# Kernel optimization log

Measured on AMD Instinct MI355X. Metric: run time of the kernel, lower is better.

The kernel has to match this reference:

```python
import jax, jax.numpy as jnp
import numpy as np
import math

DN = ('NCHW', 'OIHW', 'NCHW')

def conv2d(x, w, b=None, pad=0):
    y = jax.lax.conv_general_dilated(x, w, (1, 1), [(pad, pad), (pad, pad)], dimension_numbers=DN)
    if b is not None:
        y = y + b[None, :, None, None]
    return y

def group_norm(x, weight, bias, groups=32, eps=1e-5):
    B, C, H, W = x.shape
    xg = x.reshape(B, groups, C // groups, H, W)
    mean = xg.mean(axis=(2, 3, 4), keepdims=True)
    var = xg.var(axis=(2, 3, 4), keepdims=True)
    xg = (xg - mean) * jax.lax.rsqrt(var + eps)
    return xg.reshape(B, C, H, W) * weight[None, :, None, None] + bias[None, :, None, None]

def swish(x):
    return x * jax.nn.sigmoid(x)

def setup_inputs() -> dict:
    key = jax.random.key(0)
    ks = jax.random.split(key, 20)
    B, C, H, W = 8, 192, 48, 48
    emb = 192
    n_div = 12
    Cq = C // n_div  # 16
    s = 0.02
    return {
        'x': jax.random.normal(ks[0], (B, C, H, W), jnp.float32),
        'xe': jax.random.normal(ks[1], (B, C, H, W), jnp.float32),
        'time_emb': jax.random.normal(ks[2], (B, emb), jnp.float32),
        'gn1_w': jnp.ones((C,), jnp.float32),
        'gn1_b': jnp.zeros((C,), jnp.float32),
        'conv1_w': jax.random.normal(ks[3], (C, C, 3, 3), jnp.float32) * s,
        'conv1_b': jnp.zeros((C,), jnp.float32),
        'aff_w': jax.random.normal(ks[4], (2 * C, emb), jnp.float32) * s,
        'aff_b': jnp.zeros((2 * C,), jnp.float32),
        'gn2_w': jnp.ones((C,), jnp.float32),
        'gn2_b': jnp.zeros((C,), jnp.float32),
        'conv2_w': jax.random.normal(ks[5], (C, C, 3, 3), jnp.float32) * s,
        'conv2_b': jnp.zeros((C,), jnp.float32),
        'q_w': jax.random.normal(ks[6], (Cq, C, 1, 1), jnp.float32) * s,
        'kv_w': jax.random.normal(ks[7], (2 * Cq, C, 1, 1), jnp.float32) * s,
        'out_w': jax.random.normal(ks[8], (C, Cq, 3, 3), jnp.float32) * s,
        'out_b': jnp.zeros((C,), jnp.float32),
    }

def reference(x, xe, time_emb, gn1_w, gn1_b, conv1_w, conv1_b, aff_w, aff_b,
              gn2_w, gn2_b, conv2_w, conv2_b, q_w, kv_w, out_w, out_b):
    B, C, H, W = x.shape
    n_head, n_div = 1, 12
    head_dim = C // (n_head * n_div)

    # ----- ResnetBlock -----
    h = conv2d(swish(group_norm(x, gn1_w, gn1_b)), conv1_w, conv1_b, pad=1)
    # FeatureWiseAffine (use_affine_level=True)
    gb = time_emb @ aff_w.T + aff_b          # [B, 2C]
    gamma, beta = jnp.split(gb, 2, axis=1)   # each [B, C]
    gb_sum = 0.5 * (gamma + beta)[:, :, None, None]
    h = h + gb_sum * h + gb_sum
    h = conv2d(swish(group_norm(h, gn2_w, gn2_b)), conv2_w, conv2_b, pad=1)
    xres = h + x  # res_conv is Identity (dim == dim_out)

    # ----- CrossAttention -----
    Ye, Xe = xe.shape[-2], xe.shape[-1]
    query = conv2d(xres, q_w).reshape(B, n_head, head_dim, H, W)
    kv = conv2d(xe, kv_w).reshape(B, n_head, head_dim * 2, Ye, Xe)
    key_, value = jnp.split(kv, 2, axis=2)
    scale = 1.0 / math.sqrt(C // n_div)
    attn = jnp.einsum('bnchw,bncyx->bnhwyx', query, key_) * scale
    attn = jax.nn.softmax(attn.reshape(B, n_head, H, W, -1), axis=-1)
    attn = attn.reshape(B, n_head, H, W, Ye, Xe)
    out = jnp.einsum('bnhwyx,bncyx->bnchw', attn, value)
    out = conv2d(out.reshape(B, C // n_div, H, W), out_w, out_b, pad=1)
    return out + xres
```

## Files before the change

kernel.cpp:

```cpp
#include <hip/hip_runtime.h>
#include <hip/hip_bf16.h>

#define NB 8
#define NC 192
#define NH 48
#define NW 48
#define NP 2304
#define NGROUPS 32
#define CPG 6
#define NEMB 192
#define NCQ 16

#define PH 50
#define PWS 52
#define ACT_T_ELEMS ((size_t)NB * PH * PWS * NC)
#define AOT_ELEMS   ((size_t)NB * PH * PWS * 16)

typedef __attribute__((ext_vector_type(4))) short s16x4;
typedef __attribute__((ext_vector_type(8))) short s16x8;
typedef __attribute__((ext_vector_type(4))) float f32x4;

static __device__ inline short f2bf(float v) {
  __hip_bfloat16 h = __float2bfloat16(v);
  return *(short*)&h;
}

__global__ __launch_bounds__(256) void wprep_kernel(const float* __restrict__ w,
                                                    short* __restrict__ wbuf) {
  int i = blockIdx.x * 256 + threadIdx.x;
  if (i >= 6 * 9 * 12 * 64 * 8) return;
  int j  = i & 7;
  int l  = (i >> 3) & 63;
  int cf = (i >> 9) % 12;
  int tk = (i >> 9) / 12;
  int t  = tk % 9;
  int kc = tk / 9;
  int co = cf * 16 + (l & 15);
  int ci = kc * 32 + (l >> 4) * 8 + j;
  wbuf[i] = f2bf(w[((size_t)co * NC + ci) * 9 + t]);
}

__global__ __launch_bounds__(256) void wprep_o_kernel(const float* __restrict__ w,
                                                      short* __restrict__ wbuf) {
  int i = blockIdx.x * 256 + threadIdx.x;
  if (i >= 9 * 12 * 64 * 8) return;
  int j  = i & 7;
  int l  = (i >> 3) & 63;
  int cf = (i >> 9) % 12;
  int t  = (i >> 9) / 12;
  int co = cf * 16 + (l & 15);
  int ci = (l >> 4) * 8 + j;
  wbuf[i] = (ci < 16) ? f2bf(w[((size_t)co * 16 + ci) * 9 + t]) : (short)0;
}

__global__ __launch_bounds__(256) void affine_kernel(const float* __restrict__ emb,
                                                     const float* __restrict__ aw,
                                                     const float* __restrict__ ab,
                                                     float* __restrict__ gbsum) {
  int i = blockIdx.x * 256 + threadIdx.x;
  if (i >= NB * NC) return;
  int b = i / NC;
  int c = i - b * NC;
  const float* e  = emb + b * NEMB;
  const float* w0 = aw + c * NEMB;
  const float* w1 = aw + (c + NC) * NEMB;
  float s = 0.f;
  for (int j = 0; j < NEMB; ++j) s += e[j] * (w0[j] + w1[j]);
  gbsum[i] = 0.5f * (s + ab[c] + ab[c + NC]);
}

__global__ __launch_bounds__(256) void halo_zero_kernel(short* __restrict__ actt) {
  int b = blockIdx.y;
  int i = blockIdx.x * 256 + threadIdx.x;
  if (i >= 9600) return;
  int c4 = i % 48;
  int r  = i / 48;
  size_t off;
  if (r < 52)       off = ((size_t)0 * PWS + r) * NC;
  else if (r < 104) off = ((size_t)49 * PWS + (r - 52)) * NC;
  else if (r < 152) off = ((size_t)(r - 104 + 1) * PWS + 0) * NC;
  else              off = ((size_t)(r - 152 + 1) * PWS + 49) * NC;
  *(s16x4*)(&actt[(size_t)b * PH * PWS * NC + off + c4 * 4]) = (s16x4){0, 0, 0, 0};
}

__global__ __launch_bounds__(256) void halo_zero16_kernel(short* __restrict__ aot) {
  int b = blockIdx.x;
  for (int i = threadIdx.x; i < 784; i += 256) {
    int c4  = i & 3;
    int pos = i >> 2;
    int r, col;
    if (pos < 50)       { r = 0;  col = pos; }
    else if (pos < 100) { r = 49; col = pos - 50; }
    else if (pos < 148) { r = pos - 100 + 1; col = 0; }
    else                { r = pos - 148 + 1; col = 49; }
    *(s16x4*)(&aot[(((size_t)b * PH + r) * PWS + col) * 16 + c4 * 4]) = (s16x4){0, 0, 0, 0};
  }
}

__global__ __launch_bounds__(256) void gn_stats_kernel(const float* __restrict__ in,
                                                       float* __restrict__ stats) {
  int bg = blockIdx.x;
  const float4* p = (const float4*)(in + (size_t)bg * (CPG * NP));
  float s = 0.f, s2 = 0.f;
  for (int i = threadIdx.x; i < CPG * NP / 4; i += 256) {
    float4 v = p[i];
    s  += v.x + v.y + v.z + v.w;
    s2 += v.x * v.x + v.y * v.y + v.z * v.z + v.w * v.w;
  }
#pragma unroll
  for (int off = 32; off > 0; off >>= 1) {
    s  += __shfl_down(s, off);
    s2 += __shfl_down(s2, off);
  }
  __shared__ float red[8];
  int wave = threadIdx.x >> 6;
  if ((threadIdx.x & 63) == 0) { red[wave * 2] = s; red[wave * 2 + 1] = s2; }
  __syncthreads();
  if (threadIdx.x == 0) {
    float S  = red[0] + red[2] + red[4] + red[6];
    float S2 = red[1] + red[3] + red[5] + red[7];
    const float invN = 1.f / (float)(CPG * NP);
    float mean = S * invN;
    float var  = S2 * invN - mean * mean;
    stats[bg * 2]     = mean;
    stats[bg * 2 + 1] = rsqrtf(var + 1e-5f);
  }
}

__global__ __launch_bounds__(256) void gn_apply_t_kernel(const float* __restrict__ in,
                                                         const float* __restrict__ stats,
                                                         const float* __restrict__ gw,
                                                         const float* __restrict__ gb,
                                                         short* __restrict__ actt) {
  __shared__ float tile[48 * 193];
  int bh = blockIdx.x;
  int b = bh / NH;
  int h = bh - b * NH;
  int tid = threadIdx.x;
  for (int i = tid; i < 2304; i += 256) {
    int c = i / 12;
    int w = (i % 12) * 4;
    float4 v = *(const float4*)(in + (((size_t)b * NC + c) * NH + h) * NW + w);
    float mean = stats[(b * NGROUPS + c / CPG) * 2];
    float rstd = stats[(b * NGROUPS + c / CPG) * 2 + 1];
    float sc = rstd * gw[c];
    float sh = gb[c] - mean * sc;
    float y;
    y = v.x * sc + sh; tile[(w + 0) * 193 + c] = y / (1.f + __expf(-y));
    y = v.y * sc + sh; tile[(w + 1) * 193 + c] = y / (1.f + __expf(-y));
    y = v.z * sc + sh; tile[(w + 2) * 193 + c] = y / (1.f + __expf(-y));
    y = v.w * sc + sh; tile[(w + 3) * 193 + c] = y / (1.f + __expf(-y));
  }
  __syncthreads();
  short* dst = actt + (((size_t)b * PH + h + 1) * PWS + 1) * NC;
  for (int i = tid; i < 2304; i += 256) {
    int w  = i / 48;
    int c4 = (i - w * 48) * 4;
    s16x4 o;
    o.x = f2bf(tile[w * 193 + c4 + 0]);
    o.y = f2bf(tile[w * 193 + c4 + 1]);
    o.z = f2bf(tile[w * 193 + c4 + 2]);
    o.w = f2bf(tile[w * 193 + c4 + 3]);
    *(s16x4*)(dst + (size_t)w * NC + c4) = o;
  }
}

template <bool AFFINE, bool RESID>
__global__ __launch_bounds__(256) void conv_mfma_kernel(const short* __restrict__ actt,
                                                        const short* __restrict__ wbuf,
                                                        const float* __restrict__ bias,
                                                        const float* __restrict__ gbsum,
                                                        const float* __restrict__ resid,
                                                        float* __restrict__ out) {
  __shared__ short S[4][50][40];
  int bs = blockIdx.x;
  int b = bs / 24;
  int strip = bs - b * 24;
  int coB = blockIdx.y;
  int h0 = strip * 2;
  int tid = threadIdx.x;
  int lane = tid & 63, wave = tid >> 6;
  int wy = wave >> 1, wx = wave & 1;
  int g8 = (lane >> 4) * 8;

  f32x4 acc[2][3];
#pragma unroll
  for (int m = 0; m < 2; ++m)
#pragma unroll
    for (int f = 0; f < 3; ++f) acc[m][f] = (f32x4){0.f, 0.f, 0.f, 0.f};

  const size_t actbase = ((size_t)b * PH + h0) * PWS * NC;

  for (int kc = 0; kc < 6; ++kc) {
    __syncthreads();
    for (int i = tid; i < 800; i += 256) {
      int ci8 = i & 3;
      int rc  = i >> 2;
      int col = rc % 50, r = rc / 50;
      const s16x8* src = (const s16x8*)(actt + actbase + ((size_t)r * PWS + col) * NC +
                                        kc * 32 + ci8 * 8);
      *(s16x8*)(&S[r][col][ci8 * 8]) = *src;
    }
    __syncthreads();
#pragma unroll
    for (int t = 0; t < 9; ++t) {
      int ky = t / 3, kx = t - ky * 3;
      const short* wp = wbuf + ((((size_t)kc * 9 + t) * 12 + (coB * 4 + wy * 2)) * 64 + lane) * 8;
      s16x8 a0 = *(const s16x8*)wp;
      s16x8 a1 = *(const s16x8*)(wp + 64 * 8);
      int row = wx + ky;
#pragma unroll
      for (int f = 0; f < 3; ++f) {
        int col = f * 16 + (lane & 15) + kx;
        s16x8 bf = *(const s16x8*)(&S[row][col][g8]);
        acc[0][f] = __builtin_amdgcn_mfma_f32_16x16x32_bf16(a0, bf, acc[0][f], 0, 0, 0);
        acc[1][f] = __builtin_amdgcn_mfma_f32_16x16x32_bf16(a1, bf, acc[1][f], 0, 0, 0);
      }
    }
  }
  int hout = h0 + wx;
#pragma unroll
  for (int m = 0; m < 2; ++m) {
    int co0 = coB * 64 + wy * 32 + m * 16;
#pragma unroll
    for (int r = 0; r < 4; ++r) {
      int co = co0 + (lane >> 4) * 4 + r;
      float bv = bias[co];
      float s = AFFINE ? gbsum[b * NC + co] : 0.f;
#pragma unroll
      for (int f = 0; f < 3; ++f) {
        int w = f * 16 + (lane & 15);
        size_t o = (((size_t)b * NC + co) * NH + hout) * NW + w;
        float v = acc[m][f][r] + bv;
        if (AFFINE) v = v * (1.f + s) + s;
        if (RESID) v += resid[o];
        out[o] = v;
      }
    }
  }
}

__global__ __launch_bounds__(256) void out_conv_mfma_kernel(const short* __restrict__ aot,
                                                            const short* __restrict__ wbuf,
                                                            const float* __restrict__ bias,
                                                            float* __restrict__ out) {
  __shared__ short S[4][50][40];
  int bs = blockIdx.x;
  int b = bs / 24;
  int strip = bs - b * 24;
  int coB = blockIdx.y;
  int h0 = strip * 2;
  int tid = threadIdx.x;
  int lane = tid & 63, wave = tid >> 6;
  int wy = wave >> 1, wx = wave & 1;
  int g8 = (lane >> 4) * 8;

  f32x4 acc[2][3];
#pragma unroll
  for (int m = 0; m < 2; ++m)
#pragma unroll
    for (int f = 0; f < 3; ++f) acc[m][f] = (f32x4){0.f, 0.f, 0.f, 0.f};

  const size_t base = ((size_t)b * PH + h0) * PWS * 16;
  for (int i = tid; i < 800; i += 256) {
    int ci8 = i & 3;
    int rc  = i >> 2;
    int col = rc % 50, r = rc / 50;
    s16x8 v = (s16x8){0, 0, 0, 0, 0, 0, 0, 0};
    if (ci8 < 2)
      v = *(const s16x8*)(aot + base + ((size_t)r * PWS + col) * 16 + ci8 * 8);
    *(s16x8*)(&S[r][col][ci8 * 8]) = v;
  }
  __syncthreads();
#pragma unroll
  for (int t = 0; t < 9; ++t) {
    int ky = t / 3, kx = t - ky * 3;
    const short* wp = wbuf + (((size_t)t * 12 + (coB * 4 + wy * 2)) * 64 + lane) * 8;
    s16x8 a0 = *(const s16x8*)wp;
    s16x8 a1 = *(const s16x8*)(wp + 64 * 8);
    int row = wx + ky;
#pragma unroll
    for (int f = 0; f < 3; ++f) {
      int col = f * 16 + (lane & 15) + kx;
      s16x8 bf = *(const s16x8*)(&S[row][col][g8]);
      acc[0][f] = __builtin_amdgcn_mfma_f32_16x16x32_bf16(a0, bf, acc[0][f], 0, 0, 0);
      acc[1][f] = __builtin_amdgcn_mfma_f32_16x16x32_bf16(a1, bf, acc[1][f], 0, 0, 0);
    }
  }
  int hout = h0 + wx;
#pragma unroll
  for (int m = 0; m < 2; ++m) {
    int co0 = coB * 64 + wy * 32 + m * 16;
#pragma unroll
    for (int r = 0; r < 4; ++r) {
      int co = co0 + (lane >> 4) * 4 + r;
      float bv = bias[co];
#pragma unroll
      for (int f = 0; f < 3; ++f) {
        int w = f * 16 + (lane & 15);
        size_t o = (((size_t)b * NC + co) * NH + hout) * NW + w;
        out[o] = acc[m][f][r] + bv + out[o];
      }
    }
  }
}

template <int NOUT>
__global__ __launch_bounds__(256) void prep_partial_kernel(const float* __restrict__ X,
                                                           const float* __restrict__ W,
                                                           float* __restrict__ part) {
  __shared__ float wl[NOUT][64];
  int pt = blockIdx.x, ch = blockIdx.y, b = blockIdx.z;
  for (int i = threadIdx.x; i < NOUT * 64; i += 256) {
    int o = i >> 6, c = i & 63;
    wl[o][c] = W[o * NC + ch * 64 + c];
  }
  __syncthreads();
  int p = pt * 256 + threadIdx.x;
  const float* ip = X + ((size_t)b * NC + ch * 64) * NP + p;
  float acc[NOUT];
#pragma unroll
  for (int o = 0; o < NOUT; ++o) acc[o] = 0.f;
#pragma unroll 8
  for (int ci = 0; ci < 64; ++ci) {
    float xv = ip[(size_t)ci * NP];
#pragma unroll
    for (int o = 0; o < NOUT; ++o) acc[o] += xv * wl[o][ci];
  }
  float* op = part + ((size_t)(ch * NB + b) * NOUT) * NP + p;
#pragma unroll
  for (int o = 0; o < NOUT; ++o) op[(size_t)o * NP] = acc[o];
}

__global__ __launch_bounds__(256) void prep_pack_kernel(const float* __restrict__ pq,
                                                        const float* __restrict__ pkv,
                                                        short* __restrict__ Qb,
                                                        short* __restrict__ Kb,
                                                        short* __restrict__ VTb) {
  __shared__ short QL[16][264], KL[16][264];
  int pt = blockIdx.x, b = blockIdx.y;
  int tp = threadIdx.x;
  int p  = pt * 256 + tp;
  const float SC = 0.36067376022224085f;
#pragma unroll
  for (int o = 0; o < 16; ++o) {
    float s = pq[((size_t)(0 * NB + b) * 16 + o) * NP + p] +
              pq[((size_t)(1 * NB + b) * 16 + o) * NP + p] +
              pq[((size_t)(2 * NB + b) * 16 + o) * NP + p];
    QL[o][tp] = f2bf(s * SC);
  }
#pragma unroll
  for (int o = 0; o < 32; ++o) {
    float s = pkv[((size_t)(0 * NB + b) * 32 + o) * NP + p] +
              pkv[((size_t)(1 * NB + b) * 32 + o) * NP + p] +
              pkv[((size_t)(2 * NB + b) * 32 + o) * NP + p];
    if (o < 16) KL[o][tp] = f2bf(s);
    else VTb[((size_t)b * 16 + (o - 16)) * NP + p] = f2bf(s);
  }
  __syncthreads();
  short* qp = Qb + ((size_t)b * NP + p) * 32;
  short* kp = Kb + ((size_t)b * NP + p) * 32;
#pragma unroll
  for (int o4 = 0; o4 < 4; ++o4) {
    s16x4 vq = {QL[o4 * 4 + 0][tp], QL[o4 * 4 + 1][tp], QL[o4 * 4 + 2][tp], QL[o4 * 4 + 3][tp]};
    s16x4 vk = {KL[o4 * 4 + 0][tp], KL[o4 * 4 + 1][tp], KL[o4 * 4 + 2][tp], KL[o4 * 4 + 3][tp]};
    *(s16x4*)(qp + o4 * 4) = vq;
    *(s16x4*)(kp + o4 * 4) = vk;
    *(s16x4*)(qp + 16 + o4 * 4) = (s16x4){0, 0, 0, 0};
    *(s16x4*)(kp + 16 + o4 * 4) = (s16x4){0, 0, 0, 0};
  }
}

__global__ __launch_bounds__(1024) void attn_mfma_kernel(const short* __restrict__ Qb,
                                                         const short* __restrict__ Kb,
                                                         const short* __restrict__ VTb,
                                                         short* __restrict__ aot) {
  __shared__ float PM[4][4][64], PL[4][4][64];
  __shared__ f32x4 PA[4][4][64];
  int b    = blockIdx.y;
  int tid  = threadIdx.x;
  int lane = tid & 63;
  int w    = tid >> 6;
  int qg   = w & 3, ks = w >> 2;
  int q0   = blockIdx.x * 64 + qg * 16;
  int g    = lane >> 4;
  int ql   = lane & 15;

  s16x8 qfrag = *(const s16x8*)(Qb + ((size_t)b * NP + q0 + ql) * 32 + g * 8);

  int r0 = 8 * (ql >> 2) + (ql & 3);
  const short* Kbase = Kb + (size_t)b * NP * 32 + g * 8;
  const short* Vbase = VTb + ((size_t)b * 16 + ql) * NP;

  f32x4 acc = {0.f, 0.f, 0.f, 0.f};
  float m = -1e30f, l = 0.f;

  int kk = ks * 576;
  s16x8 kf0 = *(const s16x8*)(Kbase + (size_t)(kk + r0) * 32);
  s16x8 kf1 = *(const s16x8*)(Kbase + (size_t)(kk + r0 + 4) * 32);
  s16x8 vf  = *(const s16x8*)(Vbase + kk + g * 8);

  for (int step = 0; step < 18; ++step) {
    int kn = (step < 17) ? kk + 32 : ks * 576;
    s16x8 nk0 = *(const s16x8*)(Kbase + (size_t)(kn + r0) * 32);
    s16x8 nk1 = *(const s16x8*)(Kbase + (size_t)(kn + r0 + 4) * 32);
    s16x8 nv  = *(const s16x8*)(Vbase + kn + g * 8);

    f32x4 z = {0.f, 0.f, 0.f, 0.f};
    f32x4 s0 = __builtin_amdgcn_mfma_f32_16x16x32_bf16(kf0, qfrag, z, 0, 0, 0);
    f32x4 s1 = __builtin_amdgcn_mfma_f32_16x16x32_bf16(kf1, qfrag, z, 0, 0, 0);

    float tm = fmaxf(fmaxf(fmaxf(s0[0], s0[1]), fmaxf(s0[2], s0[3])),
                     fmaxf(fmaxf(s1[0], s1[1]), fmaxf(s1[2], s1[3])));
    if (!__all(tm <= m + 8.0f)) {
      tm = fmaxf(tm, __shfl_xor(tm, 16, 64));
      tm = fmaxf(tm, __shfl_xor(tm, 32, 64));
      float mn = fmaxf(m, tm);
      float corr = exp2f(m - mn);
      m = mn;
      l *= corr;
      acc[0] *= corr; acc[1] *= corr; acc[2] *= corr; acc[3] *= corr;
    }
    float p0 = exp2f(s0[0] - m), p1 = exp2f(s0[1] - m);
    float p2 = exp2f(s0[2] - m), p3 = exp2f(s0[3] - m);
    float p4 = exp2f(s1[0] - m), p5 = exp2f(s1[1] - m);
    float p6 = exp2f(s1[2] - m), p7 = exp2f(s1[3] - m);
    l += ((p0 + p1) + (p2 + p3)) + ((p4 + p5) + (p6 + p7));

    s16x8 pf;
    pf[0] = f2bf(p0); pf[1] = f2bf(p1); pf[2] = f2bf(p2); pf[3] = f2bf(p3);
    pf[4] = f2bf(p4); pf[5] = f2bf(p5); pf[6] = f2bf(p6); pf[7] = f2bf(p7);
    acc = __builtin_amdgcn_mfma_f32_16x16x32_bf16(vf, pf, acc, 0, 0, 0);

    kf0 = nk0; kf1 = nk1; vf = nv; kk = kn;
  }
  PM[ks][qg][lane] = m;
  PL[ks][qg][lane] = l;
  PA[ks][qg][lane] = acc;
  __syncthreads();
  if (ks == 0) {
    float M = PM[0][qg][lane];
#pragma unroll
    for (int k = 1; k < 4; ++k) M = fmaxf(M, PM[k][qg][lane]);
    float L = 0.f;
    f32x4 o = {0.f, 0.f, 0.f, 0.f};
#pragma unroll
    for (int k = 0; k < 4; ++k) {
      float c = exp2f(PM[k][qg][lane] - M);
      L += PL[k][qg][lane] * c;
      f32x4 a = PA[k][qg][lane];
      o[0] += a[0] * c; o[1] += a[1] * c; o[2] += a[2] * c; o[3] += a[3] * c;
    }
    L += __shfl_xor(L, 16, 64);
    L += __shfl_xor(L, 32, 64);
    float inv = 1.f / L;
    int q = q0 + ql;
    int h = q / NW, wcol = q - h * NW;
    s16x4 ov;
    ov.x = f2bf(o[0] * inv);
    ov.y = f2bf(o[1] * inv);
    ov.z = f2bf(o[2] * inv);
    ov.w = f2bf(o[3] * inv);
    *(s16x4*)(aot + (((size_t)b * PH + h + 1) * PWS + wcol + 1) * 16 + g * 4) = ov;
  }
}

extern "C" void kernel_launch(void* const* d_in, const int* in_sizes, int n_in,
                              void* d_out, int out_size, void* d_ws, size_t ws_size,
                              hipStream_t stream) {
  const float* x      = (const float*)d_in[0];
  const float* xe     = (const float*)d_in[1];
  const float* temb   = (const float*)d_in[2];
  const float* gn1w   = (const float*)d_in[3];
  const float* gn1b   = (const float*)d_in[4];
  const float* conv1w = (const float*)d_in[5];
  const float* conv1b = (const float*)d_in[6];
  const float* affw   = (const float*)d_in[7];
  const float* affb   = (const float*)d_in[8];
  const float* gn2w   = (const float*)d_in[9];
  const float* gn2b   = (const float*)d_in[10];
  const float* conv2w = (const float*)d_in[11];
  const float* conv2b = (const float*)d_in[12];
  const float* qw     = (const float*)d_in[13];
  const float* kvw    = (const float*)d_in[14];
  const float* outw   = (const float*)d_in[15];
  const float* outb   = (const float*)d_in[16];
  float* out = (float*)d_out;
  float* ws  = (float*)d_ws;

  float* gbsum  = ws;
  float* stats  = gbsum + NB * NC;
  float* partQ  = stats + 512;
  float* partKV = partQ + (size_t)3 * NB * 16 * NP;
  short* wbuf1  = (short*)(partKV + (size_t)3 * NB * 32 * NP);
  short* wbuf2  = wbuf1 + (size_t)6 * 9 * 12 * 64 * 8;
  short* wbufo  = wbuf2 + (size_t)6 * 9 * 12 * 64 * 8;
  short* actt   = wbufo + (size_t)9 * 12 * 64 * 8;
  short* Qb     = actt + ACT_T_ELEMS;
  short* Kb     = Qb + (size_t)NB * NP * 32;
  short* VTb    = Kb + (size_t)NB * NP * 32;
  short* aot    = VTb + (size_t)NB * 16 * NP;

  wprep_kernel<<<1296, 256, 0, stream>>>(conv1w, wbuf1);
  wprep_kernel<<<1296, 256, 0, stream>>>(conv2w, wbuf2);
  wprep_o_kernel<<<216, 256, 0, stream>>>(outw, wbufo);
  affine_kernel<<<6, 256, 0, stream>>>(temb, affw, affb, gbsum);
  halo_zero_kernel<<<dim3(38, NB), 256, 0, stream>>>(actt);
  halo_zero16_kernel<<<NB, 256, 0, stream>>>(aot);
  prep_partial_kernel<32><<<dim3(9, 3, NB), 256, 0, stream>>>(xe, kvw, partKV);

  gn_stats_kernel<<<NB * NGROUPS, 256, 0, stream>>>(x, stats);
  gn_apply_t_kernel<<<NB * NH, 256, 0, stream>>>(x, stats, gn1w, gn1b, actt);
  conv_mfma_kernel<true, false><<<dim3(NB * 24, 3), 256, 0, stream>>>(
      actt, wbuf1, conv1b, gbsum, nullptr, out);
  gn_stats_kernel<<<NB * NGROUPS, 256, 0, stream>>>(out, stats);
  gn_apply_t_kernel<<<NB * NH, 256, 0, stream>>>(out, stats, gn2w, gn2b, actt);
  conv_mfma_kernel<false, true><<<dim3(NB * 24, 3), 256, 0, stream>>>(
      actt, wbuf2, conv2b, nullptr, x, out);

  prep_partial_kernel<16><<<dim3(9, 3, NB), 256, 0, stream>>>(out, qw, partQ);
  prep_pack_kernel<<<dim3(9, NB), 256, 0, stream>>>(partQ, partKV, Qb, Kb, VTb);
  attn_mfma_kernel<<<dim3(36, NB), 1024, 0, stream>>>(Qb, Kb, VTb, aot);
  out_conv_mfma_kernel<<<dim3(NB * 24, 3), 256, 0, stream>>>(aot, wbufo, outb, out);
}
```

Measured before the change: 300.8 us.

## Compute Q/KV 1x1 projections with bf16 MFMA and split GroupNorm stats reduction

Replaces the scalar fp32 partial-sum Q/KV projection kernels and the separate pack kernel with a transpose-to-bf16 pass followed by an MFMA-based 1x1 conv that writes Q, K and V^T directly in the attention layout. The softmax scale is folded into the prepacked Q weights. GroupNorm statistics are also split across six segments per group, with a separate tiny reduce kernel, to raise parallelism. This adds extra transpose kernels and bf16 intermediate buffers, and rounds the input activations to bf16 before the projection rather than converting only the fp32 results.

```diff
diff --git a/kernel.cpp b/kernel.cpp
--- a/kernel.cpp
+++ b/kernel.cpp
@@ -51,6 +51,18 @@
   int co = cf * 16 + (l & 15);
   int ci = (l >> 4) * 8 + j;
   wbuf[i] = (ci < 16) ? f2bf(w[((size_t)co * 16 + ci) * 9 + t]) : (short)0;
+}
+
+template <int NM>
+__global__ __launch_bounds__(256) void wprep_a_kernel(const float* __restrict__ w,
+                                                      short* __restrict__ aw, float scale) {
+  int i = blockIdx.x * 256 + threadIdx.x;
+  if (i >= 6 * NM * 64 * 8) return;
+  int j = i & 7, l = (i >> 3) & 63, rest = i >> 9;
+  int m = rest % NM, kc = rest / NM;
+  int co = m * 16 + (l & 15);
+  int ci = kc * 32 + (l >> 4) * 8 + j;
+  aw[i] = f2bf(w[(size_t)co * NC + ci] * scale);
 }
 
 __global__ __launch_bounds__(256) void affine_kernel(const float* __restrict__ emb,
@@ -97,12 +109,12 @@
   }
 }
 
-__global__ __launch_bounds__(256) void gn_stats_kernel(const float* __restrict__ in,
-                                                       float* __restrict__ stats) {
-  int bg = blockIdx.x;
-  const float4* p = (const float4*)(in + (size_t)bg * (CPG * NP));
+__global__ __launch_bounds__(192) void gn_stats_part_kernel(const float* __restrict__ in,
+                                                            float* __restrict__ part) {
+  int bg = blockIdx.x, seg = blockIdx.y;
+  const float4* p = (const float4*)(in + (size_t)bg * (CPG * NP) + seg * 2304);
   float s = 0.f, s2 = 0.f;
-  for (int i = threadIdx.x; i < CPG * NP / 4; i += 256) {
+  for (int i = threadIdx.x; i < 576; i += 192) {
     float4 v = p[i];
     s  += v.x + v.y + v.z + v.w;
     s2 += v.x * v.x + v.y * v.y + v.z * v.z + v.w * v.w;
@@ -112,19 +124,30 @@
     s  += __shfl_down(s, off);
     s2 += __shfl_down(s2, off);
   }
-  __shared__ float red[8];
+  __shared__ float red[6];
   int wave = threadIdx.x >> 6;
   if ((threadIdx.x & 63) == 0) { red[wave * 2] = s; red[wave * 2 + 1] = s2; }
   __syncthreads();
   if (threadIdx.x == 0) {
-    float S  = red[0] + red[2] + red[4] + red[6];
-    float S2 = red[1] + red[3] + red[5] + red[7];
-    const float invN = 1.f / (float)(CPG * NP);
-    float mean = S * invN;
-    float var  = S2 * invN - mean * mean;
-    stats[bg * 2]     = mean;
-    stats[bg * 2 + 1] = rsqrtf(var + 1e-5f);
-  }
+    part[(bg * 6 + seg) * 2]     = red[0] + red[2] + red[4];
+    part[(bg * 6 + seg) * 2 + 1] = red[1] + red[3] + red[5];
+  }
+}
+
+__global__ __launch_bounds__(256) void gn_stats_reduce_kernel(const float* __restrict__ part,
+                                                              float* __restrict__ stats) {
+  int bg = threadIdx.x;
+  float S = 0.f, S2 = 0.f;
+#pragma unroll
+  for (int k = 0; k < 6; ++k) {
+    S  += part[(bg * 6 + k) * 2];
+    S2 += part[(bg * 6 + k) * 2 + 1];
+  }
+  const float invN = 1.f / (float)(CPG * NP);
+  float mean = S * invN;
+  float var  = S2 * invN - mean * mean;
+  stats[bg * 2]     = mean;
+  stats[bg * 2 + 1] = rsqrtf(var + 1e-5f);
 }
 
 __global__ __launch_bounds__(256) void gn_apply_t_kernel(const float* __restrict__ in,
@@ -165,6 +188,73 @@
   }
 }
 
+__global__ __launch_bounds__(256) void tconv_kernel(const float* __restrict__ in,
+                                                    short* __restrict__ xT) {
+  __shared__ float tile[48 * 193];
+  int bh = blockIdx.x;
+  int b = bh / NH;
+  int h = bh - b * NH;
+  int tid = threadIdx.x;
+  for (int i = tid; i < 2304; i += 256) {
+    int c = i / 12;
+    int w = (i % 12) * 4;
+    float4 v = *(const float4*)(in + (((size_t)b * NC + c) * NH + h) * NW + w);
+    tile[(w + 0) * 193 + c] = v.x;
+    tile[(w + 1) * 193 + c] = v.y;
+    tile[(w + 2) * 193 + c] = v.z;
+    tile[(w + 3) * 193 + c] = v.w;
+  }
+  __syncthreads();
+  short* dst = xT + (size_t)(b * NP + h * NW) * NC;
+  for (int i = tid; i < 2304; i += 256) {
+    int w  = i / 48;
+    int c4 = (i - w * 48) * 4;
+    s16x4 o;
+    o.x = f2bf(tile[w * 193 + c4 + 0]);
+    o.y = f2bf(tile[w * 193 + c4 + 1]);
+    o.z = f2bf(tile[w * 193 + c4 + 2]);
+    o.w = f2bf(tile[w * 193 + c4 + 3]);
+    *(s16x4*)(dst + (size_t)w * NC + c4) = o;
+  }
+}
+
+template <int NM, bool ISKV>
+__global__ __launch_bounds__(256) void qkv_mfma_kernel(const short* __restrict__ xT,
+                                                       const short* __restrict__ aw,
+                                                       short* __restrict__ KQ,
+                                                       short* __restrict__ VTb) {
+  int b    = blockIdx.y;
+  int lane = threadIdx.x & 63;
+  int wv   = threadIdx.x >> 6;
+  int g    = lane >> 4, ql = lane & 15;
+  int p    = blockIdx.x * 64 + wv * 16 + ql;
+
+  f32x4 acc[NM];
+#pragma unroll
+  for (int m = 0; m < NM; ++m) acc[m] = (f32x4){0.f, 0.f, 0.f, 0.f};
+
+  const short* bp = xT + ((size_t)b * NP + p) * NC + g * 8;
+#pragma unroll
+  for (int kc = 0; kc < 6; ++kc) {
+    s16x8 bf = *(const s16x8*)(bp + kc * 32);
+#pragma unroll
+    for (int m = 0; m < NM; ++m) {
+      s16x8 af = *(const s16x8*)(aw + ((size_t)(kc * NM + m) * 64 + lane) * 8);
+      acc[m] = __builtin_amdgcn_mfma_f32_16x16x32_bf16(af, bf, acc[m], 0, 0, 0);
+    }
+  }
+  s16x4 o0;
+  o0.x = f2bf(acc[0][0]); o0.y = f2bf(acc[0][1]);
+  o0.z = f2bf(acc[0][2]); o0.w = f2bf(acc[0][3]);
+  *(s16x4*)(KQ + ((size_t)b * NP + p) * 32 + g * 4) = o0;
+  *(s16x4*)(KQ + ((size_t)b * NP + p) * 32 + 16 + g * 4) = (s16x4){0, 0, 0, 0};
+  if (ISKV) {
+#pragma unroll
+    for (int r = 0; r < 4; ++r)
+      VTb[((size_t)b * 16 + g * 4 + r) * NP + p] = f2bf(acc[NM - 1][r]);
+  }
+}
+
 template <bool AFFINE, bool RESID>
 __global__ __launch_bounds__(256) void conv_mfma_kernel(const short* __restrict__ actt,
                                                         const short* __restrict__ wbuf,
@@ -302,72 +392,6 @@
         out[o] = acc[m][f][r] + bv + out[o];
       }
     }
-  }
-}
-
-template <int NOUT>
-__global__ __launch_bounds__(256) void prep_partial_kernel(const float* __restrict__ X,
-                                                           const float* __restrict__ W,
-                                                           float* __restrict__ part) {
-  __shared__ float wl[NOUT][64];
-  int pt = blockIdx.x, ch = blockIdx.y, b = blockIdx.z;
-  for (int i = threadIdx.x; i < NOUT * 64; i += 256) {
-    int o = i >> 6, c = i & 63;
-    wl[o][c] = W[o * NC + ch * 64 + c];
-  }
-  __syncthreads();
-  int p = pt * 256 + threadIdx.x;
-  const float* ip = X + ((size_t)b * NC + ch * 64) * NP + p;
-  float acc[NOUT];
-#pragma unroll
-  for (int o = 0; o < NOUT; ++o) acc[o] = 0.f;
-#pragma unroll 8
-  for (int ci = 0; ci < 64; ++ci) {
-    float xv = ip[(size_t)ci * NP];
-#pragma unroll
-    for (int o = 0; o < NOUT; ++o) acc[o] += xv * wl[o][ci];
-  }
-  float* op = part + ((size_t)(ch * NB + b) * NOUT) * NP + p;
-#pragma unroll
-  for (int o = 0; o < NOUT; ++o) op[(size_t)o * NP] = acc[o];
-}
-
-__global__ __launch_bounds__(256) void prep_pack_kernel(const float* __restrict__ pq,
-                                                        const float* __restrict__ pkv,
-                                                        short* __restrict__ Qb,
-                                                        short* __restrict__ Kb,
-                                                        short* __restrict__ VTb) {
-  __shared__ short QL[16][264], KL[16][264];
-  int pt = blockIdx.x, b = blockIdx.y;
-  int tp = threadIdx.x;
-  int p  = pt * 256 + tp;
-  const float SC = 0.36067376022224085f;
-#pragma unroll
-  for (int o = 0; o < 16; ++o) {
-    float s = pq[((size_t)(0 * NB + b) * 16 + o) * NP + p] +
-              pq[((size_t)(1 * NB + b) * 16 + o) * NP + p] +
-              pq[((size_t)(2 * NB + b) * 16 + o) * NP + p];
-    QL[o][tp] = f2bf(s * SC);
-  }
-#pragma unroll
-  for (int o = 0; o < 32; ++o) {
-    float s = pkv[((size_t)(0 * NB + b) * 32 + o) * NP + p] +
-              pkv[((size_t)(1 * NB + b) * 32 + o) * NP + p] +
-              pkv[((size_t)(2 * NB + b) * 32 + o) * NP + p];
-    if (o < 16) KL[o][tp] = f2bf(s);
-    else VTb[((size_t)b * 16 + (o - 16)) * NP + p] = f2bf(s);
-  }
-  __syncthreads();
-  short* qp = Qb + ((size_t)b * NP + p) * 32;
-  short* kp = Kb + ((size_t)b * NP + p) * 32;
-#pragma unroll
-  for (int o4 = 0; o4 < 4; ++o4) {
-    s16x4 vq = {QL[o4 * 4 + 0][tp], QL[o4 * 4 + 1][tp], QL[o4 * 4 + 2][tp], QL[o4 * 4 + 3][tp]};
-    s16x4 vk = {KL[o4 * 4 + 0][tp], KL[o4 * 4 + 1][tp], KL[o4 * 4 + 2][tp], KL[o4 * 4 + 3][tp]};
-    *(s16x4*)(qp + o4 * 4) = vq;
-    *(s16x4*)(kp + o4 * 4) = vk;
-    *(s16x4*)(qp + 16 + o4 * 4) = (s16x4){0, 0, 0, 0};
-    *(s16x4*)(kp + 16 + o4 * 4) = (s16x4){0, 0, 0, 0};
   }
 }
 
@@ -488,38 +512,49 @@
   float* out = (float*)d_out;
   float* ws  = (float*)d_ws;
 
+  const float SC = 0.36067376022224085f;
+
   float* gbsum  = ws;
   float* stats  = gbsum + NB * NC;
-  float* partQ  = stats + 512;
-  float* partKV = partQ + (size_t)3 * NB * 16 * NP;
-  short* wbuf1  = (short*)(partKV + (size_t)3 * NB * 32 * NP);
+  float* gnpart = stats + 512;
+  short* wbuf1  = (short*)(gnpart + 3072);
   short* wbuf2  = wbuf1 + (size_t)6 * 9 * 12 * 64 * 8;
   short* wbufo  = wbuf2 + (size_t)6 * 9 * 12 * 64 * 8;
-  short* actt   = wbufo + (size_t)9 * 12 * 64 * 8;
+  short* awq    = wbufo + (size_t)9 * 12 * 64 * 8;
+  short* awkv   = awq + 3072;
+  short* actt   = awkv + 6144;
   short* Qb     = actt + ACT_T_ELEMS;
   short* Kb     = Qb + (size_t)NB * NP * 32;
   short* VTb    = Kb + (size_t)NB * NP * 32;
   short* aot    = VTb + (size_t)NB * 16 * NP;
+  short* xeT    = aot + AOT_ELEMS;
+  short* xrT    = xeT + (size_t)NB * NP * NC;
 
   wprep_kernel<<<1296, 256, 0, stream>>>(conv1w, wbuf1);
   wprep_kernel<<<1296, 256, 0, stream>>>(conv2w, wbuf2);
   wprep_o_kernel<<<216, 256, 0, stream>>>(outw, wbufo);
+  wprep_a_kernel<1><<<12, 256, 0, stream>>>(qw, awq, SC);
+  wprep_a_kernel<2><<<24, 256, 0, stream>>>(kvw, awkv, 1.0f);
   affine_kernel<<<6, 256, 0, stream>>>(temb, affw, affb, gbsum);
   halo_zero_kernel<<<dim3(38, NB), 256, 0, stream>>>(actt);
   halo_zero16_kernel<<<NB, 256, 0, stream>>>(aot);
-  prep_partial_kernel<32><<<dim3(9, 3, NB), 256, 0, stream>>>(xe, kvw, partKV);
-
-  gn_stats_kernel<<<NB * NGROUPS, 256, 0, stream>>>(x, stats);
+
+  tconv_kernel<<<NB * NH, 256, 0, stream>>>(xe, xeT);
+  qkv_mfma_kernel<2, true><<<dim3(36, NB), 256, 0, stream>>>(xeT, awkv, Kb, VTb);
+
+  gn_stats_part_kernel<<<dim3(NB * NGROUPS, 6), 192, 0, stream>>>(x, gnpart);
+  gn_stats_reduce_kernel<<<1, 256, 0, stream>>>(gnpart, stats);
   gn_apply_t_kernel<<<NB * NH, 256, 0, stream>>>(x, stats, gn1w, gn1b, actt);
   conv_mfma_kernel<true, false><<<dim3(NB * 24, 3), 256, 0, stream>>>(
       actt, wbuf1, conv1b, gbsum, nullptr, out);
-  gn_stats_kernel<<<NB * NGROUPS, 256, 0, stream>>>(out, stats);
+  gn_stats_part_kernel<<<dim3(NB * NGROUPS, 6), 192, 0, stream>>>(out, gnpart);
+  gn_stats_reduce_kernel<<<1, 256, 0, stream>>>(gnpart, stats);
   gn_apply_t_kernel<<<NB * NH, 256, 0, stream>>>(out, stats, gn2w, gn2b, actt);
   conv_mfma_kernel<false, true><<<dim3(NB * 24, 3), 256, 0, stream>>>(
       actt, wbuf2, conv2b, nullptr, x, out);
 
-  prep_partial_kernel<16><<<dim3(9, 3, NB), 256, 0, stream>>>(out, qw, partQ);
-  prep_pack_kernel<<<dim3(9, NB), 256, 0, stream>>>(partQ, partKV, Qb, Kb, VTb);
+  tconv_kernel<<<NB * NH, 256, 0, stream>>>(out, xrT);
+  qkv_mfma_kernel<1, false><<<dim3(36, NB), 256, 0, stream>>>(xrT, awq, Qb, nullptr);
   attn_mfma_kernel<<<dim3(36, NB), 1024, 0, stream>>>(Qb, Kb, VTb, aot);
   out_conv_mfma_kernel<<<dim3(NB * 24, 3), 256, 0, stream>>>(aot, wbufo, outb, out);
 }
```

After: 275.8 us. 1.09x faster.
